# Kernel tuning notes

Measured on AMD Instinct MI355X. Metric: run time of the kernel, lower is better.

## Reference

```python
import jax, jax.numpy as jnp
import numpy as np
from jax import lax

WINDOW = 11
C1 = (0.01 * 1) ** 2
C2 = (0.03 * 1) ** 2


def setup_inputs() -> dict:
    key = jax.random.key(0)
    kx, ky = jax.random.split(key)
    x = jax.random.uniform(kx, (8, 3, 512, 512), dtype=jnp.float32)
    y = jax.random.uniform(ky, (8, 3, 512, 512), dtype=jnp.float32)
    return {"x": x, "y": y}


def _window_sum(a):
    # sum over every overlapping WINDOW x WINDOW patch (stride 1, valid)
    return lax.reduce_window(a, 0.0, lax.add,
                             (1, 1, WINDOW, WINDOW),
                             (1, 1, 1, 1), 'VALID')


def reference(x, y):
    # x, y: [B, C, H, W] images in [0, 1]
    n = float(WINDOW * WINDOW)
    sx = _window_sum(x)
    sy = _window_sum(y)
    sxx = _window_sum(x * x)
    syy = _window_sum(y * y)
    sxy = _window_sum(x * y)
    mx = sx / n
    my = sy / n
    # unbiased variance / covariance (matches torch var(unbiased=True) and
    # the bessel-corrected covariance in the original)
    vx = (sxx - n * mx * mx) / (n - 1.0)
    vy = (syy - n * my * my) / (n - 1.0)
    cov = (sxy - n * mx * my) / (n - 1.0)
    ssim = (2.0 * mx * my + C1) * (2.0 * cov + C2) / (
        (mx * mx + my * my + C1) * (vx + vy + C2))
    # original averages over windows (dim 0) and channels (dim 2) -> per-batch
    return (1.0 - ssim.mean(axis=(1, 2, 3))) / 2.0
```

## Files before the change

### kernel.cpp

```cpp
#include <hip/hip_runtime.h>

#define WINDOW 11
#define H 512
#define W 512
#define OH 502
#define OW 502
#define NCH 3
#define BATCH 8
#define RSTRIPE 33
#define NSTRIPES 16
#define NGRP 5
#define GRPW 118
#define WAVES_PER_IMG (NSTRIPES * NGRP)
#define NWAVES (BATCH * NCH * WAVES_PER_IMG)
#define WAVES_PER_BATCH (NCH * WAVES_PER_IMG)
#define NXCD 8
#define CHUNK (NWAVES / NXCD)

#define NPIX_PER_BATCH (3.0f * 502.0f * 502.0f)

template <int CTRL, int RM>
__device__ __forceinline__ float scan_step(float x) {
    int s = __builtin_amdgcn_update_dpp(0, __builtin_bit_cast(int, x),
                                        CTRL, RM, 0xf, false);
    return x + __builtin_bit_cast(float, s);
}
__device__ __forceinline__ float wave_iscan(float x) {
    x = scan_step<0x111, 0xf>(x);
    x = scan_step<0x112, 0xf>(x);
    x = scan_step<0x114, 0xf>(x);
    x = scan_step<0x118, 0xf>(x);
    x = scan_step<0x142, 0xa>(x);
    x = scan_step<0x143, 0xc>(x);
    return x;
}

__device__ __forceinline__ float ssim_from(float sx, float sy, float s2, float sxy) {
    const float n = 121.0f;
    const float inv_n = 1.0f / 121.0f;
    const float inv_nm1 = 1.0f / 120.0f;
    const float c1 = 1e-4f;
    const float c2 = 9e-4f;
    float mx  = sx * inv_n;
    float my  = sy * inv_n;
    float mxy = mx * my;
    float m2  = mx * mx + my * my;
    float cov = (sxy - n * mxy) * inv_nm1;
    float v2  = (s2  - n * m2)  * inv_nm1;
    float num = (2.f * mxy + c1) * (2.f * cov + c2);
    float den = (m2 + c1) * (v2 + c2);
    return num * __builtin_amdgcn_rcpf(den);
}

__global__ __launch_bounds__(64) void ssim_main(const float* __restrict__ x,
                                                const float* __restrict__ y,
                                                float* __restrict__ partials) {
    const int lane = threadIdx.x & 63;

    const int wg    = blockIdx.x;
    const int w_lin = (wg % NXCD) * CHUNK + wg / NXCD;

    const int img = w_lin / WAVES_PER_IMG;
    const int rem = w_lin % WAVES_PER_IMG;
    const int grp = rem / NSTRIPES;
    const int rs  = rem % NSTRIPES;

    const int i0 = rs * RSTRIPE;
    const int i1 = min(i0 + RSTRIPE, OH);
    const int cstart = grp * GRPW;
    const int outw   = min(GRPW, OW - cstart);
    const int c0 = min(cstart + 2 * lane, W - 2);
    const bool tapActive = (2 * lane < outw);

    const float* __restrict__ xc = x + (size_t)img * H * W + c0;
    const float* __restrict__ yc = y + (size_t)img * H * W + c0;

    float2 fx[11], fy[11];
    float4 v0 = make_float4(0.f, 0.f, 0.f, 0.f);
    float4 v1 = make_float4(0.f, 0.f, 0.f, 0.f);
#pragma unroll
    for (int r = 0; r < WINDOW; ++r) {
        float2 a = *(const float2*)(xc + (size_t)(i0 + r) * W);
        float2 b = *(const float2*)(yc + (size_t)(i0 + r) * W);
        fx[r] = a; fy[r] = b;
        v0.x += a.x; v0.y += b.x; v0.z += a.x * a.x + b.x * b.x; v0.w += a.x * b.x;
        v1.x += a.y; v1.y += b.y; v1.z += a.y * a.y + b.y * b.y; v1.w += a.y * b.y;
    }

    float2 nx, ny;
#define LDNEW(j) do {                                                \
        int jc_ = min((j), H - 1);                                   \
        nx = *(const float2*)(xc + (size_t)jc_ * W);                 \
        ny = *(const float2*)(yc + (size_t)jc_ * W);                 \
    } while (0)

#define SLIDE(u) do {                                                 \
        v0.x += nx.x - fx[u].x;                                       \
        v0.y += ny.x - fy[u].x;                                       \
        v0.z += nx.x * nx.x + ny.x * ny.x                             \
              - fx[u].x * fx[u].x - fy[u].x * fy[u].x;                \
        v0.w += nx.x * ny.x - fx[u].x * fy[u].x;                      \
        v1.x += nx.y - fx[u].y;                                       \
        v1.y += ny.y - fy[u].y;                                       \
        v1.z += nx.y * nx.y + ny.y * ny.y                             \
              - fx[u].y * fx[u].y - fy[u].y * fy[u].y;                \
        v1.w += nx.y * ny.y - fx[u].y * fy[u].y;                      \
        fx[u] = nx; fy[u] = ny;                                       \
    } while (0)

    float acc = 0.f;

#define COMPUTE(rowActive) do {                                               \
        float Tx = v0.x + v1.x, Ty = v0.y + v1.y;                             \
        float Tz = v0.z + v1.z, Tw = v0.w + v1.w;                             \
        float Sx = wave_iscan(Tx), Sy = wave_iscan(Ty);                       \
        float Sz = wave_iscan(Tz), Sw = wave_iscan(Tw);                       \
        int src = lane + 5;                                                   \
        float Ax = __shfl(Sx, src, 64), Ay = __shfl(Sy, src, 64);             \
        float Az = __shfl(Sz, src, 64), Aw = __shfl(Sw, src, 64);             \
        float Bx = __shfl(v1.x, src, 64), By = __shfl(v1.y, src, 64);         \
        float Bz = __shfl(v1.z, src, 64), Bw = __shfl(v1.w, src, 64);         \
        if (tapActive & (rowActive)) {                                        \
            acc += ssim_from(Ax - Bx - Sx + Tx, Ay - By - Sy + Ty,            \
                             Az - Bz - Sz + Tz, Aw - Bw - Sw + Tw);           \
            acc += ssim_from(Ax - Sx + v1.x, Ay - Sy + v1.y,                  \
                             Az - Sz + v1.z, Aw - Sw + v1.w);                 \
        }                                                                     \
    } while (0)

    LDNEW(i0 + WINDOW);
    for (int base = i0; base < i1; base += 11) {
#pragma unroll
        for (int u = 0; u < 11; ++u) {
            const int i = base + u;
            COMPUTE(i < i1);
            SLIDE(u);
            LDNEW(i + WINDOW + 1);
        }
    }

    for (int off = 32; off > 0; off >>= 1)
        acc += __shfl_down(acc, off, 64);
    if (lane == 0) partials[w_lin] = acc;
}

__global__ __launch_bounds__(256) void ssim_reduce(const float* __restrict__ partials,
                                                   float* __restrict__ out) {
    const int b = blockIdx.x;
    const int t = threadIdx.x;
    float s = 0.f;
    if (t < WAVES_PER_BATCH)
        s = partials[b * WAVES_PER_BATCH + t];
    for (int off = 32; off > 0; off >>= 1)
        s += __shfl_down(s, off, 64);
    __shared__ float red[4];
    int wid = t >> 6, lane = t & 63;
    if (lane == 0) red[wid] = s;
    __syncthreads();
    if (t == 0) {
        float tot = (red[0] + red[1]) + (red[2] + red[3]);
        out[b] = (1.0f - tot / NPIX_PER_BATCH) * 0.5f;
    }
}

extern "C" void kernel_launch(void* const* d_in, const int* in_sizes, int n_in,
                              void* d_out, int out_size, void* d_ws, size_t ws_size,
                              hipStream_t stream) {
    const float* x = (const float*)d_in[0];
    const float* y = (const float*)d_in[1];
    float* out      = (float*)d_out;
    float* partials = (float*)d_ws;

    ssim_main<<<NWAVES, 64, 0, stream>>>(x, y, partials);
    ssim_reduce<<<BATCH, 256, 0, stream>>>(partials, out);
}
```

Before: 26.89 us.

## Replace DPP prefix scan with shuffle ladder and pack math into float2 vectors

The horizontal 11-wide window sum across lanes was a full 6-step DPP inclusive scan plus shuffles. It is now a short ladder of shuffles (offsets 1, 2, 4, 5) that builds only the 5- and 6-lane partial sums needed for the even and odd output columns. Vertical sliding sums and the SSIM formula use two-wide float vectors so the compiler can emit packed FP32 instructions. The branch on active taps becomes a select. This trades cheap DPP ops for more ds_bpermute-style shuffles, which may have higher latency.

```diff
diff --git a/kernel.cpp b/kernel.cpp
--- a/kernel.cpp
+++ b/kernel.cpp
@@ -19,38 +19,7 @@
 
 #define NPIX_PER_BATCH (3.0f * 502.0f * 502.0f)
 
-template <int CTRL, int RM>
-__device__ __forceinline__ float scan_step(float x) {
-    int s = __builtin_amdgcn_update_dpp(0, __builtin_bit_cast(int, x),
-                                        CTRL, RM, 0xf, false);
-    return x + __builtin_bit_cast(float, s);
-}
-__device__ __forceinline__ float wave_iscan(float x) {
-    x = scan_step<0x111, 0xf>(x);
-    x = scan_step<0x112, 0xf>(x);
-    x = scan_step<0x114, 0xf>(x);
-    x = scan_step<0x118, 0xf>(x);
-    x = scan_step<0x142, 0xa>(x);
-    x = scan_step<0x143, 0xc>(x);
-    return x;
-}
-
-__device__ __forceinline__ float ssim_from(float sx, float sy, float s2, float sxy) {
-    const float n = 121.0f;
-    const float inv_n = 1.0f / 121.0f;
-    const float inv_nm1 = 1.0f / 120.0f;
-    const float c1 = 1e-4f;
-    const float c2 = 9e-4f;
-    float mx  = sx * inv_n;
-    float my  = sy * inv_n;
-    float mxy = mx * my;
-    float m2  = mx * mx + my * my;
-    float cov = (sxy - n * mxy) * inv_nm1;
-    float v2  = (s2  - n * m2)  * inv_nm1;
-    float num = (2.f * mxy + c1) * (2.f * cov + c2);
-    float den = (m2 + c1) * (v2 + c2);
-    return num * __builtin_amdgcn_rcpf(den);
-}
+typedef float v2f __attribute__((ext_vector_type(2)));
 
 __global__ __launch_bounds__(64) void ssim_main(const float* __restrict__ x,
                                                 const float* __restrict__ y,
@@ -75,57 +44,69 @@
     const float* __restrict__ xc = x + (size_t)img * H * W + c0;
     const float* __restrict__ yc = y + (size_t)img * H * W + c0;
 
-    float2 fx[11], fy[11];
-    float4 v0 = make_float4(0.f, 0.f, 0.f, 0.f);
-    float4 v1 = make_float4(0.f, 0.f, 0.f, 0.f);
+    const int s1 = lane + 1, s2 = lane + 2, s4 = lane + 4, s5 = lane + 5;
+
+    v2f fx[11], fy[11];
+    v2f Qx = 0.f, Qy = 0.f, Qz = 0.f, Qw = 0.f;
 #pragma unroll
     for (int r = 0; r < WINDOW; ++r) {
-        float2 a = *(const float2*)(xc + (size_t)(i0 + r) * W);
-        float2 b = *(const float2*)(yc + (size_t)(i0 + r) * W);
+        v2f a = *(const v2f*)(xc + (size_t)(i0 + r) * W);
+        v2f b = *(const v2f*)(yc + (size_t)(i0 + r) * W);
         fx[r] = a; fy[r] = b;
-        v0.x += a.x; v0.y += b.x; v0.z += a.x * a.x + b.x * b.x; v0.w += a.x * b.x;
-        v1.x += a.y; v1.y += b.y; v1.z += a.y * a.y + b.y * b.y; v1.w += a.y * b.y;
+        Qx += a;
+        Qy += b;
+        Qz += a * a + b * b;
+        Qw += a * b;
     }
 
-    float2 nx, ny;
+    v2f nx, ny;
 #define LDNEW(j) do {                                                \
         int jc_ = min((j), H - 1);                                   \
-        nx = *(const float2*)(xc + (size_t)jc_ * W);                 \
-        ny = *(const float2*)(yc + (size_t)jc_ * W);                 \
+        nx = *(const v2f*)(xc + (size_t)jc_ * W);                    \
+        ny = *(const v2f*)(yc + (size_t)jc_ * W);                    \
     } while (0)
 
 #define SLIDE(u) do {                                                 \
-        v0.x += nx.x - fx[u].x;                                       \
-        v0.y += ny.x - fy[u].x;                                       \
-        v0.z += nx.x * nx.x + ny.x * ny.x                             \
-              - fx[u].x * fx[u].x - fy[u].x * fy[u].x;                \
-        v0.w += nx.x * ny.x - fx[u].x * fy[u].x;                      \
-        v1.x += nx.y - fx[u].y;                                       \
-        v1.y += ny.y - fy[u].y;                                       \
-        v1.z += nx.y * nx.y + ny.y * ny.y                             \
-              - fx[u].y * fx[u].y - fy[u].y * fy[u].y;                \
-        v1.w += nx.y * ny.y - fx[u].y * fy[u].y;                      \
+        Qx += nx - fx[u];                                             \
+        Qy += ny - fy[u];                                             \
+        Qz += nx * nx + ny * ny - fx[u] * fx[u] - fy[u] * fy[u];      \
+        Qw += nx * ny - fx[u] * fy[u];                                \
         fx[u] = nx; fy[u] = ny;                                       \
     } while (0)
 
     float acc = 0.f;
 
+#define LADDER(T, q0, q1, We, Wo) do {                                \
+        float U1 = T + __shfl(T, s1, 64);                             \
+        float U2 = U1 + __shfl(U1, s2, 64);                           \
+        float S5 = U2 + __shfl(T, s4, 64);                            \
+        float S6 = S5 + __shfl(T, s5, 64);                            \
+        We = S5 + __shfl(q0, s5, 64);                                 \
+        Wo = S6 - T + q1;                                             \
+    } while (0)
+
 #define COMPUTE(rowActive) do {                                               \
-        float Tx = v0.x + v1.x, Ty = v0.y + v1.y;                             \
-        float Tz = v0.z + v1.z, Tw = v0.w + v1.w;                             \
-        float Sx = wave_iscan(Tx), Sy = wave_iscan(Ty);                       \
-        float Sz = wave_iscan(Tz), Sw = wave_iscan(Tw);                       \
-        int src = lane + 5;                                                   \
-        float Ax = __shfl(Sx, src, 64), Ay = __shfl(Sy, src, 64);             \
-        float Az = __shfl(Sz, src, 64), Aw = __shfl(Sw, src, 64);             \
-        float Bx = __shfl(v1.x, src, 64), By = __shfl(v1.y, src, 64);         \
-        float Bz = __shfl(v1.z, src, 64), Bw = __shfl(v1.w, src, 64);         \
-        if (tapActive & (rowActive)) {                                        \
-            acc += ssim_from(Ax - Bx - Sx + Tx, Ay - By - Sy + Ty,            \
-                             Az - Bz - Sz + Tz, Aw - Bw - Sw + Tw);           \
-            acc += ssim_from(Ax - Sx + v1.x, Ay - Sy + v1.y,                  \
-                             Az - Sz + v1.z, Aw - Sw + v1.w);                 \
-        }                                                                     \
+        float Tx = Qx.x + Qx.y, Ty = Qy.x + Qy.y;                             \
+        float Tz = Qz.x + Qz.y, Tw = Qw.x + Qw.y;                             \
+        float Wex, Wox, Wey, Woy, Wez, Woz, Wew, Wow;                         \
+        LADDER(Tx, Qx.x, Qx.y, Wex, Wox);                                     \
+        LADDER(Ty, Qy.x, Qy.y, Wey, Woy);                                     \
+        LADDER(Tz, Qz.x, Qz.y, Wez, Woz);                                     \
+        LADDER(Tw, Qw.x, Qw.y, Wew, Wow);                                     \
+        v2f Wx = {Wex, Wox}, Wy = {Wey, Woy};                                 \
+        v2f Wz = {Wez, Woz}, Ww = {Wew, Wow};                                 \
+                             \
+        v2f mx  = Wx * (1.0f / 121.0f);                                       \
+        v2f my  = Wy * (1.0f / 121.0f);                                       \
+        v2f mxy = mx * my;                                                    \
+        v2f m2  = mx * mx + my * my;                                          \
+        v2f cov = (Ww - 121.0f * mxy) * (1.0f / 120.0f);                      \
+        v2f vv  = (Wz - 121.0f * m2)  * (1.0f / 120.0f);                      \
+        v2f num = (2.0f * mxy + 1e-4f) * (2.0f * cov + 9e-4f);                \
+        v2f den = (m2 + 1e-4f) * (vv + 9e-4f);                                \
+        float r = num.x * __builtin_amdgcn_rcpf(den.x)                        \
+                + num.y * __builtin_amdgcn_rcpf(den.y);                       \
+        acc += (tapActive & (rowActive)) ? r : 0.f;                           \
     } while (0)
 
     LDNEW(i0 + WINDOW);
```

Measured after the change: 28.87 us. 1.07x slower.
